# Performance work log

Measured on AMD Instinct MI355X. Metric: run time of the kernel, lower is better.

Reference implementation:

```python
import jax, jax.numpy as jnp
import numpy as np

B, T, NG = 1024, 16, 23            # clips, window, nodes per timestep graph
H, IN, L, C = 64, 8, 20, 3         # hidden, input_dim, num_layers, classes
E_PER = 256                        # edges per graph
NUM_GRAPHS = B * T                 # 16384
N = NUM_GRAPHS * NG                # 376832 nodes
E = NUM_GRAPHS * E_PER             # 4194304 edges
LN_EPS = 1e-5


def setup_inputs() -> dict:
    key = jax.random.key(0)
    ks = jax.random.split(key, 16)
    s = 0.05
    x = jax.random.normal(ks[0], (N, IN), jnp.float32)
    # intra-graph random edges: global_id = graph_id * NG + local_id
    gid = jnp.repeat(jnp.arange(NUM_GRAPHS, dtype=jnp.int32), E_PER)
    src_l = jax.random.randint(ks[1], (E,), 0, NG, dtype=jnp.int32)
    dst_l = jax.random.randint(ks[2], (E,), 0, NG, dtype=jnp.int32)
    edge_index = jnp.stack([gid * NG + src_l, gid * NG + dst_l])
    batch = jnp.repeat(jnp.arange(NUM_GRAPHS, dtype=jnp.int32), NG)
    return {
        "x": x,
        "edge_index": edge_index,
        "batch": batch,
        "W_enc": jax.random.normal(ks[3], (IN, H), jnp.float32) * s,
        "b_enc": jnp.zeros((H,), jnp.float32),
        "ln_g": jnp.ones((L, H), jnp.float32),
        "ln_b": jnp.zeros((L, H), jnp.float32),
        "W_rel": jax.random.normal(ks[4], (L, H, H), jnp.float32) * s,
        "b_rel": jnp.zeros((L, H), jnp.float32),
        "W_root": jax.random.normal(ks[5], (L, H, H), jnp.float32) * s,
        "pos": jax.random.normal(ks[6], (1, T, H), jnp.float32) * 0.02,
        "W1": jax.random.normal(ks[7], (H, H), jnp.float32) * s,
        "b1": jnp.zeros((H,), jnp.float32),
        "W2": jax.random.normal(ks[8], (H, C), jnp.float32) * s,
        "b2": jnp.zeros((C,), jnp.float32),
    }


def _layer_norm(h, g, b):
    mu = jnp.mean(h, axis=-1, keepdims=True)
    var = jnp.mean(jnp.square(h - mu), axis=-1, keepdims=True)
    return (h - mu) * jax.lax.rsqrt(var + LN_EPS) * g + b


def reference(x, edge_index, batch, W_enc, b_enc, ln_g, ln_b, W_rel, b_rel,
              W_root, pos, W1, b1, W2, b2):
    src, dst = edge_index[0], edge_index[1]
    h = x @ W_enc + b_enc                      # node encoder, [N, H]

    # DeepGCNLayer block='res+': out = x + GraphConv(relu(LN(x)))
    # GraphConv: lin_rel(sum_{j->i} z_j) + lin_root(z)  (aggr='add')
    def step(h, p):
        g, b, Wr, br, Wo = p
        z = jax.nn.relu(_layer_norm(h, g, b))  # dropout = identity (eval)
        agg = jax.ops.segment_sum(z[src], dst, num_segments=N)
        return h + agg @ Wr + br + z @ Wo, None

    h, _ = jax.lax.scan(step, h, (ln_g, ln_b, W_rel, b_rel, W_root))

    # global mean pool (each graph has exactly NG nodes)
    pooled = jax.ops.segment_sum(h, batch, num_segments=NUM_GRAPHS) / NG
    xt = pooled.reshape(B, T, H) + pos[:, :T, :]
    v = jnp.mean(xt, axis=1)                   # temporal 'pool'
    h1 = jax.nn.relu(v @ W1 + b1)
    return h1 @ W2 + b2                        # [B, C]
```

## Files before the change

### kernel.cpp

```cpp
#include <hip/hip_runtime.h>
#include <hip/hip_bf16.h>

#define NGRAPH 16384
#define NPAIR  (NGRAPH / 2)
#define NG     23
#define PCOLS  46
#define HD     64
#define INF    8
#define LAYERS 20
#define EDGES_PER 256
#define E_TOT  (NGRAPH * EDGES_PER)
#define BATCH  1024
#define TWIN   16
#define CLS    3

#define NS 64

typedef __attribute__((ext_vector_type(8))) short s8v;
typedef __attribute__((ext_vector_type(4))) float f4v;
typedef __attribute__((ext_vector_type(2))) float f2v;

union FragU { unsigned u[4]; s8v v; };

__device__ inline f2v vlo(f4v v) { return (f2v){v[0], v[1]}; }
__device__ inline f2v vhi(f4v v) { return (f2v){v[2], v[3]}; }

__device__ inline unsigned pk2_bf16(f2v v) {
  __hip_bfloat162 b = __float22bfloat162_rn(make_float2(v[0], v[1]));
  unsigned r;
  __builtin_memcpy(&r, &b, sizeof(r));
  return r;
}

__device__ inline f2v max0(f2v v) {
#if defined(__has_builtin) && __has_builtin(__builtin_elementwise_max)
  return __builtin_elementwise_max(v, (f2v){0.f, 0.f});
#else
  return (f2v){fmaxf(v[0], 0.f), fmaxf(v[1], 0.f)};
#endif
}

__device__ inline unsigned f2bf_pk(float a, float b) {
  unsigned ua = __builtin_bit_cast(unsigned, a);
  unsigned ub = __builtin_bit_cast(unsigned, b);
  ua = ua + 0x7FFFu + ((ua >> 16) & 1u);
  ub = ub + 0x7FFFu + ((ub >> 16) & 1u);
  return (ua >> 16) | (ub & 0xFFFF0000u);
}

__global__ __launch_bounds__(256) void pack_w(const float* __restrict__ W_rel,
                                              const float* __restrict__ W_root,
                                              unsigned* __restrict__ wf) {
  const int tid = blockIdx.x * 256 + threadIdx.x;
  if (tid >= LAYERS * 2 * 4 * 2 * 64) return;
  const int lane = tid & 63, fi = tid >> 6;
  const int Kt = fi & 1, Mt = (fi >> 1) & 3, m = (fi >> 3) & 1, l = fi >> 4;
  const float* W = (m ? W_root : W_rel) + (size_t)l * HD * HD;
  const int col = lane & 15, quad = lane >> 4;
  const int jdim = Mt * 16 + col;
  unsigned pk[4];
#pragma unroll
  for (int w = 0; w < 4; ++w) {
    const int j0 = 2 * w, j1 = 2 * w + 1;
    const int d0 = ((j0 >> 2) * 2 + Kt) * 16 + quad * 4 + (j0 & 3);
    const int d1 = ((j1 >> 2) * 2 + Kt) * 16 + quad * 4 + (j1 & 3);
    pk[w] = f2bf_pk(W[(size_t)d0 * HD + jdim], W[(size_t)d1 * HD + jdim]);
  }
  uint4 q; q.x = pk[0]; q.y = pk[1]; q.z = pk[2]; q.w = pk[3];
  *(uint4*)&wf[(size_t)tid * 4] = q;
}

__global__ __launch_bounds__(256, 4) void gcn_main(
    const float* __restrict__ x, const int* __restrict__ ei,
    const unsigned* __restrict__ wf,
    const float* __restrict__ W_enc, const float* __restrict__ b_enc,
    const float* __restrict__ ln_g, const float* __restrict__ ln_b,
    const float* __restrict__ b_rel, float* __restrict__ pooled) {
  __shared__ __align__(16) unsigned short sm[4 * HD * NS];
  const int lane = threadIdx.x & 63, wv = threadIdx.x >> 6;
  const int p = blockIdx.x * 4 + wv;
  const int col = lane & 15, quad = lane >> 4;
  unsigned short* zt = sm + wv * (HD * NS);

  unsigned* cnt = (unsigned*)zt;
  for (int i = lane; i < 48 * 24; i += 64) cnt[i] = 0;
  asm volatile("s_waitcnt lgkmcnt(0)" ::: "memory");
  {
    const int ebase = p * (2 * EDGES_PER);
    const int noff = p * PCOLS;
#pragma unroll
    for (int r = 0; r < 8; ++r) {
      const int e = ebase + r * 64 + lane;
      const int s = ei[e] - noff;
      const int d = ei[E_TOT + e] - noff;
      atomicAdd(&cnt[d * 24 + (s >> 1)], 1u << ((s & 1) * 16));
    }
  }
  asm volatile("s_waitcnt lgkmcnt(0)" ::: "memory");

  FragU adjB[3][2];
#pragma unroll
  for (int Nt = 0; Nt < 3; ++Nt) {
    const int dst = col + 16 * Nt;
    const bool dok = dst < PCOLS;
#pragma unroll
    for (int Kt = 0; Kt < 2; ++Kt)
#pragma unroll
      for (int w = 0; w < 4; ++w) {
        const int s0 = Kt * 32 + quad * 8 + 2 * w;
        float v0 = 0.f, v1 = 0.f;
        if (dok && s0 < PCOLS) {
          const unsigned rd = cnt[dst * 24 + (s0 >> 1)];
          v0 = (float)(rd & 0xffffu);
          if (s0 + 1 < PCOLS) v1 = (float)(rd >> 16);
        }
        adjB[Nt][Kt].u[w] = f2bf_pk(v0, v1);
      }
  }
  asm volatile("s_waitcnt lgkmcnt(0)" ::: "memory");

  {
    uint4 z4; z4.x = 0; z4.y = 0; z4.z = 0; z4.w = 0;
    for (int i = lane; i < (HD * NS * 2) / 16; i += 64) ((uint4*)zt)[i] = z4;
  }
  asm volatile("s_waitcnt lgkmcnt(0)" ::: "memory");

  const int c7 = (col >> 1) & 7;
  const int ra0 = col * NS + ((quad ^ c7) << 3);
  const unsigned short* zA = zt + ra0;
  const unsigned short* zB = zt + (ra0 ^ 32);
  int wb[3][2];
#pragma unroll
  for (int Nt = 0; Nt < 3; ++Nt) {
    const int node = col + 16 * Nt;
    wb[Nt][0] = (quad * 4    ) * NS + (((node >> 3) ^ (quad * 2    )) << 3) + (node & 7);
    wb[Nt][1] = (quad * 4 + 2) * NS + (((node >> 3) ^ (quad * 2 + 1)) << 3) + (node & 7);
  }

  f4v acc[4][3];
  {
    const float* xg = x + (size_t)p * PCOLS * INF;
    f4v xa[3][2];
    const f4v zz = {0.f, 0.f, 0.f, 0.f};
#pragma unroll
    for (int Nt = 0; Nt < 3; ++Nt) {
      const int c = col + 16 * Nt;
      if (c < PCOLS) {
        const float* xp = xg + (size_t)c * INF;
        xa[Nt][0] = *(const f4v*)xp;
        xa[Nt][1] = *(const f4v*)(xp + 4);
      } else { xa[Nt][0] = zz; xa[Nt][1] = zz; }
    }
#pragma unroll
    for (int Mt = 0; Mt < 4; ++Mt) {
      const f4v be = *(const f4v*)(b_enc + Mt * 16 + quad * 4);
      acc[Mt][0] = be; acc[Mt][1] = be; acc[Mt][2] = be;
#pragma unroll
      for (int i = 0; i < INF; ++i) {
        const f4v we = *(const f4v*)(W_enc + i * HD + Mt * 16 + quad * 4);
        acc[Mt][0] += we * xa[0][i >> 2][i & 3];
        acc[Mt][1] += we * xa[1][i >> 2][i & 3];
        acc[Mt][2] += we * xa[2][i >> 2][i & 3];
      }
    }
  }

#pragma unroll 1
  for (int l = 0; l < LAYERS; ++l) {
    const unsigned* wbase = wf + (size_t)l * (2 * 4 * 2 * 64 * 4);

    float mu[3], rs[3];
    {
      float sh[3], qh[3];
#pragma unroll
      for (int Nt = 0; Nt < 3; ++Nt) {
        f2v t = vlo(acc[0][Nt]) + vhi(acc[0][Nt]);
        t += vlo(acc[1][Nt]); t += vhi(acc[1][Nt]);
        t += vlo(acc[2][Nt]); t += vhi(acc[2][Nt]);
        t += vlo(acc[3][Nt]); t += vhi(acc[3][Nt]);
        f2v u = vlo(acc[0][Nt]) * vlo(acc[0][Nt]);
        u += vhi(acc[0][Nt]) * vhi(acc[0][Nt]);
        u += vlo(acc[1][Nt]) * vlo(acc[1][Nt]);
        u += vhi(acc[1][Nt]) * vhi(acc[1][Nt]);
        u += vlo(acc[2][Nt]) * vlo(acc[2][Nt]);
        u += vhi(acc[2][Nt]) * vhi(acc[2][Nt]);
        u += vlo(acc[3][Nt]) * vlo(acc[3][Nt]);
        u += vhi(acc[3][Nt]) * vhi(acc[3][Nt]);
        sh[Nt] = t[0] + t[1];
        qh[Nt] = u[0] + u[1];
      }
#pragma unroll
      for (int Nt = 0; Nt < 3; ++Nt) { sh[Nt] += __shfl_xor(sh[Nt], 16); qh[Nt] += __shfl_xor(qh[Nt], 16); }
#pragma unroll
      for (int Nt = 0; Nt < 3; ++Nt) { sh[Nt] += __shfl_xor(sh[Nt], 32); qh[Nt] += __shfl_xor(qh[Nt], 32); }
#pragma unroll
      for (int Nt = 0; Nt < 3; ++Nt) {
        mu[Nt] = sh[Nt] * (1.0f / HD);
        float var = fmaf(qh[Nt], (1.0f / HD), -mu[Nt] * mu[Nt]);
        var = fmaxf(var, 0.f);
        rs[Nt] = rsqrtf(var + 1e-5f);
      }
    }

    FragU zpk[2][3];
#pragma unroll
    for (int Kt = 0; Kt < 2; ++Kt) {
#pragma unroll
      for (int hi = 0; hi < 2; ++hi) {
        const int Mt = Kt + 2 * hi;
        const f4v gf  = *(const f4v*)(ln_g + l * HD + Mt * 16 + quad * 4);
        const f4v bfv = *(const f4v*)(ln_b + l * HD + Mt * 16 + quad * 4);
        const f2v gl = vlo(gf), gh = vhi(gf);
        const f2v bl = vlo(bfv), bh = vhi(bfv);
#pragma unroll
        for (int Nt = 0; Nt < 3; ++Nt) {
          const f2v sgl = gl * rs[Nt], sgh = gh * rs[Nt];
          const f2v tbl = bl - mu[Nt] * sgl, tbh = bh - mu[Nt] * sgh;
          const f2v zl = max0(vlo(acc[Mt][Nt]) * sgl + tbl);
          const f2v zh = max0(vhi(acc[Mt][Nt]) * sgh + tbh);
          zpk[Kt][Nt].u[hi * 2 + 0] = pk2_bf16(zl);
          zpk[Kt][Nt].u[hi * 2 + 1] = pk2_bf16(zh);
        }
      }
#pragma unroll
      for (int hi = 0; hi < 2; ++hi) {
        const int Mt = Kt + 2 * hi;
#pragma unroll
        for (int Nt = 0; Nt < 3; ++Nt)
#pragma unroll
          for (int r2 = 0; r2 < 2; ++r2) {
            const unsigned d = zpk[Kt][Nt].u[hi * 2 + r2];
            unsigned short* pz = zt + Mt * 1024 + wb[Nt][r2];
            pz[0]  = (unsigned short)d;
            pz[NS] = (unsigned short)(d >> 16);
          }
      }
    }

#pragma unroll
    for (int Kt = 0; Kt < 2; ++Kt)
#pragma unroll
      for (int Mt = 0; Mt < 4; ++Mt) {
        const s8v wo = *(const s8v*)&wbase[((((1 * 4) + Mt) * 2 + Kt) * 64 + lane) * 4];
#pragma unroll
        for (int Nt = 0; Nt < 3; ++Nt)
          acc[Mt][Nt] = __builtin_amdgcn_mfma_f32_16x16x32_bf16(wo, zpk[Kt][Nt].v, acc[Mt][Nt], 0, 0, 0);
      }

    asm volatile("s_waitcnt lgkmcnt(0)" ::: "memory");

    const f4v zzero = {0.f, 0.f, 0.f, 0.f};
#pragma unroll
    for (int Kt = 0; Kt < 2; ++Kt) {
      const s8v zaA0 = *(const s8v*)&zA[(Kt    ) * 1024];
      const s8v zaA1 = *(const s8v*)&zB[(Kt    ) * 1024];
      const s8v zaC0 = *(const s8v*)&zA[(Kt + 2) * 1024];
      const s8v zaC1 = *(const s8v*)&zB[(Kt + 2) * 1024];
      f4v agA[3], agC[3];
#pragma unroll
      for (int Nt = 0; Nt < 3; ++Nt) {
        agA[Nt] = __builtin_amdgcn_mfma_f32_16x16x32_bf16(zaA0, adjB[Nt][0].v, zzero, 0, 0, 0);
        agA[Nt] = __builtin_amdgcn_mfma_f32_16x16x32_bf16(zaA1, adjB[Nt][1].v, agA[Nt], 0, 0, 0);
        agC[Nt] = __builtin_amdgcn_mfma_f32_16x16x32_bf16(zaC0, adjB[Nt][0].v, zzero, 0, 0, 0);
        agC[Nt] = __builtin_amdgcn_mfma_f32_16x16x32_bf16(zaC1, adjB[Nt][1].v, agC[Nt], 0, 0, 0);
      }
      FragU apk[3];
#pragma unroll
      for (int Nt = 0; Nt < 3; ++Nt) {
        apk[Nt].u[0] = pk2_bf16(vlo(agA[Nt]));
        apk[Nt].u[1] = pk2_bf16(vhi(agA[Nt]));
        apk[Nt].u[2] = pk2_bf16(vlo(agC[Nt]));
        apk[Nt].u[3] = pk2_bf16(vhi(agC[Nt]));
      }
#pragma unroll
      for (int Mt = 0; Mt < 4; ++Mt) {
        const s8v wr = *(const s8v*)&wbase[((((0 * 4) + Mt) * 2 + Kt) * 64 + lane) * 4];
#pragma unroll
        for (int Nt = 0; Nt < 3; ++Nt)
          acc[Mt][Nt] = __builtin_amdgcn_mfma_f32_16x16x32_bf16(wr, apk[Nt].v, acc[Mt][Nt], 0, 0, 0);
      }
    }

#pragma unroll
    for (int Mt = 0; Mt < 4; ++Mt) {
      const f4v brf = *(const f4v*)(b_rel + l * HD + Mt * 16 + quad * 4);
      const f2v bl = vlo(brf), bh = vhi(brf);
#pragma unroll
      for (int Nt = 0; Nt < 3; ++Nt) {
        const f2v al = vlo(acc[Mt][Nt]) + bl;
        const f2v ah = vhi(acc[Mt][Nt]) + bh;
        acc[Mt][Nt] = (f4v){al[0], al[1], ah[0], ah[1]};
      }
    }
  }

  float* hb = (float*)zt;
  asm volatile("s_waitcnt lgkmcnt(0)" ::: "memory");
#pragma unroll
  for (int Mt = 0; Mt < 4; ++Mt)
#pragma unroll
    for (int Nt = 0; Nt < 2; ++Nt)
      *(f4v*)&hb[(col + 16 * Nt) * HD + Mt * 16 + quad * 4] = acc[Mt][Nt];
  asm volatile("s_waitcnt lgkmcnt(0)" ::: "memory");
  float sA = 0.f, sB = 0.f;
#pragma unroll
  for (int c = 0; c < NG; ++c) sA += hb[c * HD + lane];
#pragma unroll
  for (int c = NG; c < 32; ++c) sB += hb[c * HD + lane];
  asm volatile("s_waitcnt lgkmcnt(0)" ::: "memory");
#pragma unroll
  for (int Mt = 0; Mt < 4; ++Mt)
    *(f4v*)&hb[col * HD + Mt * 16 + quad * 4] = acc[Mt][2];
  asm volatile("s_waitcnt lgkmcnt(0)" ::: "memory");
#pragma unroll
  for (int c = 0; c < PCOLS - 32; ++c) sB += hb[c * HD + lane];
  pooled[(size_t)(2 * p) * HD + lane] = sA;
  pooled[(size_t)(2 * p + 1) * HD + lane] = sB;
}

__global__ __launch_bounds__(64) void head(
    const float* __restrict__ pooled, const float* __restrict__ pos,
    const float* __restrict__ W1, const float* __restrict__ b1,
    const float* __restrict__ W2, const float* __restrict__ b2,
    float* __restrict__ out) {
  __shared__ float sv[HD];
  __shared__ float sh1[HD];
  const int b = blockIdx.x, k = threadIdx.x;
  float v = 0.f;
#pragma unroll
  for (int tt = 0; tt < TWIN; ++tt) v += pooled[((size_t)(b * TWIN + tt)) * HD + k];
  float p = 0.f;
#pragma unroll
  for (int tt = 0; tt < TWIN; ++tt) p += pos[tt * HD + k];
  v = v * (1.0f / (NG * TWIN)) + p * (1.0f / TWIN);
  sv[k] = v;
  __syncthreads();
  float a = b1[k];
#pragma unroll
  for (int kk = 0; kk < HD; ++kk) a = fmaf(sv[kk], W1[kk * HD + k], a);
  a = fmaxf(a, 0.f);
  sh1[k] = a;
  __syncthreads();
  if (k < CLS) {
    float o = b2[k];
#pragma unroll
    for (int kk = 0; kk < HD; ++kk) o = fmaf(sh1[kk], W2[kk * CLS + k], o);
    out[(size_t)b * CLS + k] = o;
  }
}

extern "C" void kernel_launch(void* const* d_in, const int* in_sizes, int n_in,
                              void* d_out, int out_size, void* d_ws, size_t ws_size,
                              hipStream_t stream) {
  const float* x      = (const float*)d_in[0];
  const int*   ei     = (const int*)  d_in[1];
  const float* W_enc  = (const float*)d_in[3];
  const float* b_enc  = (const float*)d_in[4];
  const float* ln_g   = (const float*)d_in[5];
  const float* ln_b   = (const float*)d_in[6];
  const float* W_rel  = (const float*)d_in[7];
  const float* b_rel  = (const float*)d_in[8];
  const float* W_root = (const float*)d_in[9];
  const float* pos    = (const float*)d_in[10];
  const float* W1     = (const float*)d_in[11];
  const float* b1     = (const float*)d_in[12];
  const float* W2     = (const float*)d_in[13];
  const float* b2     = (const float*)d_in[14];
  float* out = (float*)d_out;

  char* p = (char*)d_ws;
  unsigned* wfrag  = (unsigned*)p;  p += (size_t)LAYERS * 2 * 4 * 2 * 64 * 16;
  float*    pooled = (float*)p;

  pack_w  <<<80, 256, 0, stream>>>(W_rel, W_root, wfrag);
  gcn_main<<<NPAIR / 4, 256, 0, stream>>>(x, ei, wfrag, W_enc, b_enc,
                                          ln_g, ln_b, b_rel, pooled);
  head    <<<BATCH, 64, 0, stream>>>(pooled, pos, W1, b1, W2, b2, out);
}
```

Before: 422.1 us.

## Precompute adjacency MFMA fragments in separate kernel and reload per layer

Moves the per-pair adjacency count construction (LDS atomics, conversion to bf16 fragments) out of the main GCN kernel into a new build_padj kernel that writes packed fragments to workspace. The main kernel then reloads the six adjacency fragments from global memory inside each layer instead of keeping them live in registers for all 20 layers. This is meant to cut register pressure in gcn_main, possibly allowing higher occupancy or less spilling. In exchange it adds a kernel launch, about 50 MB of extra global writes and reads, and repeated per-layer global loads that will likely be served from cache.

```diff
diff --git a/kernel.cpp b/kernel.cpp
--- a/kernel.cpp
+++ b/kernel.cpp
@@ -70,8 +70,51 @@
   *(uint4*)&wf[(size_t)tid * 4] = q;
 }
 
+__global__ __launch_bounds__(256) void build_padj(const int* __restrict__ ei,
+                                                  unsigned* __restrict__ adjf) {
+  __shared__ unsigned cnt[4][48 * 24];
+  const int lane = threadIdx.x & 63, wv = threadIdx.x >> 6;
+  const int p = blockIdx.x * 4 + wv;
+  const int col = lane & 15, quad = lane >> 4;
+  unsigned* c = cnt[wv];
+  for (int i = lane; i < 48 * 24; i += 64) c[i] = 0;
+  asm volatile("s_waitcnt lgkmcnt(0)" ::: "memory");
+  const int ebase = p * (2 * EDGES_PER);
+  const int noff = p * PCOLS;
+#pragma unroll
+  for (int r = 0; r < 8; ++r) {
+    const int e = ebase + r * 64 + lane;
+    const int s = ei[e] - noff;
+    const int d = ei[E_TOT + e] - noff;
+    atomicAdd(&c[d * 24 + (s >> 1)], 1u << ((s & 1) * 16));
+  }
+  asm volatile("s_waitcnt lgkmcnt(0)" ::: "memory");
+#pragma unroll
+  for (int Nt = 0; Nt < 3; ++Nt) {
+    const int dst = col + 16 * Nt;
+    const bool dok = dst < PCOLS;
+#pragma unroll
+    for (int Kt = 0; Kt < 2; ++Kt) {
+      unsigned pk[4];
+#pragma unroll
+      for (int w = 0; w < 4; ++w) {
+        const int s0 = Kt * 32 + quad * 8 + 2 * w;
+        float v0 = 0.f, v1 = 0.f;
+        if (dok && s0 < PCOLS) {
+          const unsigned rd = c[dst * 24 + (s0 >> 1)];
+          v0 = (float)(rd & 0xffffu);
+          if (s0 + 1 < PCOLS) v1 = (float)(rd >> 16);
+        }
+        pk[w] = f2bf_pk(v0, v1);
+      }
+      uint4 q; q.x = pk[0]; q.y = pk[1]; q.z = pk[2]; q.w = pk[3];
+      ((uint4*)adjf)[((size_t)p * 6 + Nt * 2 + Kt) * 64 + lane] = q;
+    }
+  }
+}
+
 __global__ __launch_bounds__(256, 4) void gcn_main(
-    const float* __restrict__ x, const int* __restrict__ ei,
+    const float* __restrict__ x, const unsigned* __restrict__ adjf,
     const unsigned* __restrict__ wf,
     const float* __restrict__ W_enc, const float* __restrict__ b_enc,
     const float* __restrict__ ln_g, const float* __restrict__ ln_b,
@@ -82,48 +125,14 @@
   const int col = lane & 15, quad = lane >> 4;
   unsigned short* zt = sm + wv * (HD * NS);
 
-  unsigned* cnt = (unsigned*)zt;
-  for (int i = lane; i < 48 * 24; i += 64) cnt[i] = 0;
-  asm volatile("s_waitcnt lgkmcnt(0)" ::: "memory");
-  {
-    const int ebase = p * (2 * EDGES_PER);
-    const int noff = p * PCOLS;
-#pragma unroll
-    for (int r = 0; r < 8; ++r) {
-      const int e = ebase + r * 64 + lane;
-      const int s = ei[e] - noff;
-      const int d = ei[E_TOT + e] - noff;
-      atomicAdd(&cnt[d * 24 + (s >> 1)], 1u << ((s & 1) * 16));
-    }
-  }
-  asm volatile("s_waitcnt lgkmcnt(0)" ::: "memory");
-
-  FragU adjB[3][2];
-#pragma unroll
-  for (int Nt = 0; Nt < 3; ++Nt) {
-    const int dst = col + 16 * Nt;
-    const bool dok = dst < PCOLS;
-#pragma unroll
-    for (int Kt = 0; Kt < 2; ++Kt)
-#pragma unroll
-      for (int w = 0; w < 4; ++w) {
-        const int s0 = Kt * 32 + quad * 8 + 2 * w;
-        float v0 = 0.f, v1 = 0.f;
-        if (dok && s0 < PCOLS) {
-          const unsigned rd = cnt[dst * 24 + (s0 >> 1)];
-          v0 = (float)(rd & 0xffffu);
-          if (s0 + 1 < PCOLS) v1 = (float)(rd >> 16);
-        }
-        adjB[Nt][Kt].u[w] = f2bf_pk(v0, v1);
-      }
-  }
-  asm volatile("s_waitcnt lgkmcnt(0)" ::: "memory");
-
   {
     uint4 z4; z4.x = 0; z4.y = 0; z4.z = 0; z4.w = 0;
     for (int i = lane; i < (HD * NS * 2) / 16; i += 64) ((uint4*)zt)[i] = z4;
   }
   asm volatile("s_waitcnt lgkmcnt(0)" ::: "memory");
+
+  const uint4* ap  = (const uint4*)adjf + (size_t)p * 384 + lane;
+  const uint4* ap4 = ap + 256;
 
   const int c7 = (col >> 1) & 7;
   const int ra0 = col * NS + ((quad ^ c7) << 3);
@@ -247,6 +256,13 @@
           acc[Mt][Nt] = __builtin_amdgcn_mfma_f32_16x16x32_bf16(wo, zpk[Kt][Nt].v, acc[Mt][Nt], 0, 0, 0);
       }
 
+    FragU adjB[3][2];
+#pragma unroll
+    for (int idx = 0; idx < 4; ++idx)
+      adjB[idx >> 1][idx & 1].v = *(const s8v*)(ap + idx * 64);
+    adjB[2][0].v = *(const s8v*)(ap4);
+    adjB[2][1].v = *(const s8v*)(ap4 + 64);
+
     asm volatile("s_waitcnt lgkmcnt(0)" ::: "memory");
 
     const f4v zzero = {0.f, 0.f, 0.f, 0.f};
@@ -256,21 +272,17 @@
       const s8v zaA1 = *(const s8v*)&zB[(Kt    ) * 1024];
       const s8v zaC0 = *(const s8v*)&zA[(Kt + 2) * 1024];
       const s8v zaC1 = *(const s8v*)&zB[(Kt + 2) * 1024];
-      f4v agA[3], agC[3];
+      FragU apk[3];
 #pragma unroll
       for (int Nt = 0; Nt < 3; ++Nt) {
-        agA[Nt] = __builtin_amdgcn_mfma_f32_16x16x32_bf16(zaA0, adjB[Nt][0].v, zzero, 0, 0, 0);
-        agA[Nt] = __builtin_amdgcn_mfma_f32_16x16x32_bf16(zaA1, adjB[Nt][1].v, agA[Nt], 0, 0, 0);
-        agC[Nt] = __builtin_amdgcn_mfma_f32_16x16x32_bf16(zaC0, adjB[Nt][0].v, zzero, 0, 0, 0);
-        agC[Nt] = __builtin_amdgcn_mfma_f32_16x16x32_bf16(zaC1, adjB[Nt][1].v, agC[Nt], 0, 0, 0);
-      }
-      FragU apk[3];
-#pragma unroll
-      for (int Nt = 0; Nt < 3; ++Nt) {
-        apk[Nt].u[0] = pk2_bf16(vlo(agA[Nt]));
-        apk[Nt].u[1] = pk2_bf16(vhi(agA[Nt]));
-        apk[Nt].u[2] = pk2_bf16(vlo(agC[Nt]));
-        apk[Nt].u[3] = pk2_bf16(vhi(agC[Nt]));
+        f4v agA = __builtin_amdgcn_mfma_f32_16x16x32_bf16(zaA0, adjB[Nt][0].v, zzero, 0, 0, 0);
+        agA     = __builtin_amdgcn_mfma_f32_16x16x32_bf16(zaA1, adjB[Nt][1].v, agA,   0, 0, 0);
+        f4v agC = __builtin_amdgcn_mfma_f32_16x16x32_bf16(zaC0, adjB[Nt][0].v, zzero, 0, 0, 0);
+        agC     = __builtin_amdgcn_mfma_f32_16x16x32_bf16(zaC1, adjB[Nt][1].v, agC,   0, 0, 0);
+        apk[Nt].u[0] = pk2_bf16(vlo(agA));
+        apk[Nt].u[1] = pk2_bf16(vhi(agA));
+        apk[Nt].u[2] = pk2_bf16(vlo(agC));
+        apk[Nt].u[3] = pk2_bf16(vhi(agC));
       }
 #pragma unroll
       for (int Mt = 0; Mt < 4; ++Mt) {
@@ -368,12 +380,14 @@
   const float* b2     = (const float*)d_in[14];
   float* out = (float*)d_out;
 
-  char* p = (char*)d_ws;
-  unsigned* wfrag  = (unsigned*)p;  p += (size_t)LAYERS * 2 * 4 * 2 * 64 * 16;
-  float*    pooled = (float*)p;
-
-  pack_w  <<<80, 256, 0, stream>>>(W_rel, W_root, wfrag);
-  gcn_main<<<NPAIR / 4, 256, 0, stream>>>(x, ei, wfrag, W_enc, b_enc,
-                                          ln_g, ln_b, b_rel, pooled);
-  head    <<<BATCH, 64, 0, stream>>>(pooled, pos, W1, b1, W2, b2, out);
-}
+  char* pp = (char*)d_ws;
+  unsigned* wfrag   = (unsigned*)pp;  pp += (size_t)LAYERS * 2 * 4 * 2 * 64 * 16;
+  unsigned* adjfrag = (unsigned*)pp;  pp += (size_t)NPAIR * 6 * 64 * 16;
+  float*    pooled  = (float*)pp;
+
+  pack_w    <<<80, 256, 0, stream>>>(W_rel, W_root, wfrag);
+  build_padj<<<NPAIR / 4, 256, 0, stream>>>(ei, adjfrag);
+  gcn_main  <<<NPAIR / 4, 256, 0, stream>>>(x, adjfrag, wfrag, W_enc, b_enc,
+                                            ln_g, ln_b, b_rel, pooled);
+  head      <<<BATCH, 64, 0, stream>>>(pooled, pos, W1, b1, W2, b2, out);
+}
```

After: 429.0 us. About the same (+1.6%).
